# Optimization experiments

Hardware: AMD Instinct MI355X
Metric: run time of the kernel (lower is better)

## Reference

```python
import jax, jax.numpy as jnp
import numpy as np

H = 2048
N = 2_097_152
BINS = 256


def _tensor2image(x):
    # de-normalize from [-1,1]-style to [0,1] (SCGAN's tensor2image)
    return x * 0.5 + 0.5


def _cdf(vals):
    # torch.histc(vals, bins=256, min=0, max=256): unit-width bins; values here lie in [0,256)
    b = jnp.clip(jnp.floor(vals), 0, BINS - 1).astype(jnp.int32)
    hist = jnp.zeros((BINS,), jnp.float32).at[b].add(1.0)
    c = jnp.cumsum(hist)
    return c / c[BINS - 1]


def _trans_table(ref_cdf, adj_cdf):
    # table[i] = first j in 1..255 with adj[j-1] <= ref[i] <= adj[j]; else i. table[0]=0, table[255]=255.
    r = ref_cdf[:, None]                # [256,1]
    lo = adj_cdf[None, :-1]             # adj[j-1], j=1..255
    hi = adj_cdf[None, 1:]              # adj[j]
    cond = (lo <= r) & (r <= hi)        # [256,255]
    found = jnp.any(cond, axis=1)
    j_first = 1 + jnp.argmax(cond, axis=1)
    table = jnp.where(found, j_first, jnp.arange(BINS))
    table = table.at[0].set(0).at[BINS - 1].set(BINS - 1)
    return table


def _histogram_matching(dst_img, ref_img, i0, i1, i2, i3):
    dst_align = dst_img[:, i0, i1]      # [3,N]
    ref_align = ref_img[:, i2, i3]      # [3,N]
    cdf_dst = jax.vmap(_cdf)(dst_align)           # [3,256]
    cdf_ref = jax.vmap(_cdf)(ref_align)           # [3,256]
    tables = jax.vmap(_trans_table)(cdf_dst, cdf_ref)  # [3,256] int
    ix = jnp.clip(jnp.floor(dst_align), 0, BINS - 1).astype(jnp.int32)
    matched = jnp.take_along_axis(tables, ix, axis=1).astype(dst_img.dtype)  # [3,N]
    return dst_img.at[:, i0, i1].set(matched)


def setup_inputs() -> dict:
    key = jax.random.key(0)
    ks = jax.random.split(key, 9)
    return {
        "input_data": jax.random.uniform(ks[0], (1, 3, H, H), jnp.float32),
        "target_data": jax.random.uniform(ks[1], (1, 3, H, H), jnp.float32),
        "mask_src": jax.random.randint(ks[2], (1, 1, H, H), 0, 2).astype(jnp.float32),
        "mask_tar": jax.random.randint(ks[3], (1, 1, H, H), 0, 2).astype(jnp.float32),
        "idx0": jax.random.randint(ks[4], (N,), 0, H),
        "idx1": jax.random.randint(ks[5], (N,), 0, H),
        "idx2": jax.random.randint(ks[6], (N,), 0, H),
        "idx3": jax.random.randint(ks[7], (N,), 0, H),
        "ref": jax.random.uniform(ks[8], (1, 3, H, H), jnp.float32),
    }


def reference(input_data, target_data, mask_src, mask_tar, idx0, idx1, idx2, idx3, ref):
    img = _tensor2image(input_data)[0] * 255.0   # [3,H,H]
    tgt = _tensor2image(target_data)[0] * 255.0  # [3,H,H]
    rf = _tensor2image(ref)[0] * 255.0           # [3,H,H]
    m_src = jnp.broadcast_to(mask_src[0, 0], img.shape)
    m_tar = jnp.broadcast_to(mask_tar[0, 0], tgt.shape)
    input_masked = img * m_src
    target_masked = tgt * m_tar
    ref_masked = rf * m_src
    match = jax.lax.stop_gradient(
        _histogram_matching(ref_masked, target_masked, idx0, idx1, idx2, idx3)
    ) * m_src
    return jnp.mean(jnp.abs(input_masked - match))
```

## Files before the change

kernel.cpp:

```cpp
#include <hip/hip_runtime.h>

#define H 2048
#define HH (H * H)
#define NIDX 2097152
#define BINS 256
#define CH 3

#define NLIST 128
#define CAPG  139264
#define WS_HIST_DST 0
#define WS_HIST_REF 3072
#define WS_TABLE    6144
#define WS_ACC      9216
#define WS_CURS     9728
#define WS_DONE_G   10240
#define WS_DONE_L   10244
#define WS_CTRL_BYTES 16384
#define WS_SEL      16384
#define WS_ZERO_BYTES (16384 + (size_t)HH)
#define WS_BPS      (16384 + (size_t)HH)
#define WS_BPR      (WS_BPS + (size_t)HH * 4)
#define WS_LIST     (WS_BPR + (size_t)HH * 4)
#define WS_MAIN_BYTES (WS_LIST + (size_t)NLIST * CAPG * 2)

#define FB_CNT_DST  16384
#define FB_BINPACK  (16384 + (size_t)HH * 2)
#define FB_ZERO_BYTES (16384 + (size_t)HH * 2)

__device__ __forceinline__ int bin_of(float v) {
    int b = (int)floorf(v);
    return min(max(b, 0), BINS - 1);
}



#define P1_BLOCKS 512
#define P1_SPB (NIDX / P1_BLOCKS)
#define P1_CAP 96
#define PREP_BLOCKS 1024
#define PQ (HH / 4 / 4)
#define FUSE_GRID (P1_BLOCKS + PREP_BLOCKS)

__global__ __launch_bounds__(256) void prep_part_kernel(
    const float* __restrict__ mask_src, const float* __restrict__ mask_tar,
    const float* __restrict__ refimg, const float* __restrict__ tgtimg,
    unsigned int* __restrict__ bps, unsigned int* __restrict__ bpr,
    const int* __restrict__ idx0, const int* __restrict__ idx1,
    const int* __restrict__ idx2, const int* __restrict__ idx3,
    unsigned short* __restrict__ list_g, unsigned int* __restrict__ curs)
{
    __shared__ unsigned short stage[NLIST * P1_CAP];
    __shared__ unsigned int lcnt[NLIST];
    __shared__ unsigned int lbase[NLIST];

    if (blockIdx.x < P1_BLOCKS) {
        for (int i = threadIdx.x; i < NLIST; i += 256) lcnt[i] = 0u;
        __syncthreads();

        const int base4 = blockIdx.x * (P1_SPB / 4);
        #pragma unroll
        for (int r = 0; r < P1_SPB / 1024; ++r) {
            int k4 = base4 + r * 256 + threadIdx.x;
            int4 a = ((const int4*)idx0)[k4];
            int4 b = ((const int4*)idx1)[k4];
            int4 c = ((const int4*)idx2)[k4];
            int4 d = ((const int4*)idx3)[k4];
            const int pd[4] = { a.x * H + b.x, a.y * H + b.y,
                                a.z * H + b.z, a.w * H + b.w };
            const int pr[4] = { c.x * H + d.x, c.y * H + d.y,
                                c.z * H + d.z, c.w * H + d.w };
            #pragma unroll
            for (int e = 0; e < 4; ++e) {
                {
                    int l = pd[e] >> 16;
                    unsigned int pos = atomicAdd(&lcnt[l], 1u);
                    if (pos < P1_CAP) stage[l * P1_CAP + pos] = (unsigned short)(pd[e] & 0xFFFF);
                    else {
                        unsigned int g = atomicAdd(&curs[l], 1u);
                        if (g < CAPG) list_g[(size_t)l * CAPG + g] = (unsigned short)(pd[e] & 0xFFFF);
                    }
                }
                {
                    int l = 64 + (pr[e] >> 16);
                    unsigned int pos = atomicAdd(&lcnt[l], 1u);
                    if (pos < P1_CAP) stage[l * P1_CAP + pos] = (unsigned short)(pr[e] & 0xFFFF);
                    else {
                        unsigned int g = atomicAdd(&curs[l], 1u);
                        if (g < CAPG) list_g[(size_t)l * CAPG + g] = (unsigned short)(pr[e] & 0xFFFF);
                    }
                }
            }
        }
        __syncthreads();
        if (threadIdx.x < NLIST) {
            unsigned int n = min(lcnt[threadIdx.x], (unsigned int)P1_CAP);
            lbase[threadIdx.x] = atomicAdd(&curs[threadIdx.x], n);
        }
        __syncthreads();
        for (int b = 0; b < NLIST; ++b) {
            int n = (int)min(lcnt[b], (unsigned int)P1_CAP);
            unsigned int gb = lbase[b];
            for (int e = threadIdx.x; e < n; e += 256) {
                unsigned int gi = gb + e;
                if (gi < CAPG) list_g[(size_t)b * CAPG + gi] = stage[b * P1_CAP + e];
            }
        }
    } else {
        const int t = (int)(blockIdx.x - P1_BLOCKS) * 256 + threadIdx.x;
        float4 msv[4], mtv[4];
        #pragma unroll
        for (int k = 0; k < 4; ++k) {
            msv[k] = ((const float4*)mask_src)[t + k * PQ];
            mtv[k] = ((const float4*)mask_tar)[t + k * PQ];
        }
        unsigned int wsrc[4][4] = {{0u,0u,0u,0u},{0u,0u,0u,0u},{0u,0u,0u,0u},{0u,0u,0u,0u}};
        unsigned int wref[4][4] = {{0u,0u,0u,0u},{0u,0u,0u,0u},{0u,0u,0u,0u},{0u,0u,0u,0u}};
        #pragma unroll
        for (int c = 0; c < CH; ++c) {
            float4 rv[4], tv[4];
            #pragma unroll
            for (int k = 0; k < 4; ++k) {
                rv[k] = ((const float4*)(refimg + (size_t)c * HH))[t + k * PQ];
                tv[k] = ((const float4*)(tgtimg + (size_t)c * HH))[t + k * PQ];
            }
            #pragma unroll
            for (int k = 0; k < 4; ++k) {
                const float* rr = &rv[k].x;
                const float* tt = &tv[k].x;
                const float* mm = &msv[k].x;
                const float* mt2 = &mtv[k].x;
                #pragma unroll
                for (int e = 0; e < 4; ++e) {
                    float vs = (rr[e] * 0.5f + 0.5f) * 255.0f * mm[e];
                    float vt = (tt[e] * 0.5f + 0.5f) * 255.0f * mt2[e];
                    wsrc[k][e] |= ((unsigned int)bin_of(vs)) << (8 * c);
                    wref[k][e] |= ((unsigned int)bin_of(vt)) << (8 * c);
                }
            }
        }
        #pragma unroll
        for (int k = 0; k < 4; ++k) {
            uint4 os = { wsrc[k][0], wsrc[k][1], wsrc[k][2], wsrc[k][3] };
            uint4 orf = { wref[k][0], wref[k][1], wref[k][2], wref[k][3] };
            ((uint4*)bps)[t + k * PQ] = os;
            ((uint4*)bpr)[t + k * PQ] = orf;
        }
    }
}

#define G_BLOCKS 1024
__global__ __launch_bounds__(256) void gather_hist_kernel(
    const unsigned short* __restrict__ list_g, const unsigned int* __restrict__ curs,
    const unsigned int* __restrict__ bps, const unsigned int* __restrict__ bpr,
    unsigned char* __restrict__ selected,
    unsigned int* __restrict__ hist_dst, unsigned int* __restrict__ hist_ref,
    int* __restrict__ table, unsigned int* __restrict__ done)
{
    __shared__ unsigned int hh[CH * BINS];
    for (int i = threadIdx.x; i < CH * BINS; i += 256) hh[i] = 0u;
    __syncthreads();

    const int xcd  = blockIdx.x & 7;
    const int j    = blockIdx.x >> 3;
    const int bsl  = j & 15;
    const int sub  = j >> 4;
    const int side = bsl >> 3;
    const int bucket = xcd * 8 + (bsl & 7);
    const int l = side * 64 + bucket;
    const unsigned int pbase = ((unsigned int)bucket) << 16;
    const unsigned int* __restrict__ src = side ? bpr : bps;

    const unsigned int n = min(curs[l], (unsigned int)CAPG);
    const unsigned int chunk = (((n + 7u) >> 3) + 7u) & ~7u;
    const unsigned int s = (unsigned int)sub * chunk;
    const unsigned int e = min(s + chunk, n);
    const unsigned short* lbase = list_g + (size_t)l * CAPG;

    unsigned int zc = 0;
    for (unsigned int ib = s + (unsigned int)threadIdx.x * 8u; ib < e; ib += 2048u) {
        unsigned int w[8];
        unsigned int pcnt;
        if (ib + 8u <= e) {
            uint4 raw = *(const uint4*)(lbase + ib);
            const unsigned int ent[8] = {
                raw.x & 0xFFFFu, raw.x >> 16, raw.y & 0xFFFFu, raw.y >> 16,
                raw.z & 0xFFFFu, raw.z >> 16, raw.w & 0xFFFFu, raw.w >> 16 };
            #pragma unroll
            for (int k = 0; k < 8; ++k) {
                unsigned int p = pbase | ent[k];
                w[k] = src[p];
                if (side == 0) selected[p] = 1;
            }
            pcnt = 8u;
        } else {
            pcnt = e - ib;
            #pragma unroll
            for (int k = 0; k < 8; ++k) {
                if ((unsigned int)k < pcnt) {
                    unsigned int p = pbase | (unsigned int)lbase[ib + k];
                    w[k] = src[p];
                    if (side == 0) selected[p] = 1;
                } else w[k] = 0xFFFFFFFFu;
            }
        }
        #pragma unroll
        for (int k = 0; k < 8; ++k) {
            if ((unsigned int)k < pcnt) {
                unsigned int ww = w[k];
                if (ww == 0u) ++zc;
                else {
                    atomicAdd(&hh[0 * BINS + (ww & 0xFFu)], 1u);
                    atomicAdd(&hh[1 * BINS + ((ww >> 8) & 0xFFu)], 1u);
                    atomicAdd(&hh[2 * BINS + ((ww >> 16) & 0xFFu)], 1u);
                }
            }
        }
    }

    int z = (int)zc;
    #pragma unroll
    for (int off = 32; off; off >>= 1) z += __shfl_down(z, off);
    if ((threadIdx.x & 63) == 0 && z) {
        atomicAdd(&hh[0 * BINS], (unsigned int)z);
        atomicAdd(&hh[1 * BINS], (unsigned int)z);
        atomicAdd(&hh[2 * BINS], (unsigned int)z);
    }

    __syncthreads();
    unsigned int* dsthist = side ? hist_ref : hist_dst;
    for (int i = threadIdx.x; i < CH * BINS; i += 256) {
        unsigned int v = hh[i];
        if (v) atomicAdd(&dsthist[i], v);
    }

    __shared__ int is_last;
    __syncthreads();
    if (threadIdx.x == 0) {
        unsigned int t = atomicAdd(done, 1u);
        is_last = (t == gridDim.x - 1u) ? 1 : 0;
    }
    __syncthreads();
    if (!is_last) return;

    __shared__ float cd[CH * BINS];
    __shared__ float cr[CH * BINS];
    __shared__ float wpart[4];
    const int i = threadIdx.x;
    const int lane = i & 63;
    const int wave = i >> 6;

    for (int a = 0; a < 6; ++a) {
        unsigned int* h = (a < 3) ? (hist_dst + a * BINS) : (hist_ref + (a - 3) * BINS);
        float* out = (a < 3) ? (cd + a * BINS) : (cr + (a - 3) * BINS);
        float x = (float)atomicAdd(&h[i], 0u);
        #pragma unroll
        for (int off = 1; off < 64; off <<= 1) {
            float y = __shfl_up(x, off);
            if (lane >= off) x += y;
        }
        if (lane == 63) wpart[wave] = x;
        __syncthreads();
        float prefix = 0.0f;
        #pragma unroll
        for (int w = 0; w < 3; ++w) if (w < wave) prefix += wpart[w];
        x += prefix;
        float tot = wpart[0] + wpart[1] + wpart[2] + wpart[3];
        out[i] = x / tot;
        __syncthreads();
    }

    #pragma unroll
    for (int c = 0; c < CH; ++c) {
        int t;
        if (i == 0) t = 0;
        else if (i == BINS - 1) t = BINS - 1;
        else {
            float r = cd[c * BINS + i];
            int lo = 1, hi = BINS - 1;
            while (lo < hi) {
                int mid = (lo + hi) >> 1;
                if (cr[c * BINS + mid] < r) lo = mid + 1; else hi = mid;
            }
            t = (cr[c * BINS + lo - 1] <= r) ? lo : i;
        }
        table[c * BINS + i] = t;
    }
}

#define L_BLOCKS 1024
__global__ __launch_bounds__(256) void loss_sel_kernel(
    const float* __restrict__ input, const float* __restrict__ refimg,
    const float* __restrict__ mask_src, const unsigned char* __restrict__ selected,
    const int* __restrict__ table, double* __restrict__ acc,
    float* __restrict__ out_loss, unsigned int* __restrict__ done)
{
    __shared__ int tab[CH * BINS];
    for (int i = threadIdx.x; i < CH * BINS; i += 256) tab[i] = table[i];
    __syncthreads();

    const int t = blockIdx.x * 256 + threadIdx.x;
    float4 mv[4];
    uchar4 sv[4];
    #pragma unroll
    for (int k = 0; k < 4; ++k) {
        mv[k] = ((const float4*)mask_src)[t + k * PQ];
        sv[k] = ((const uchar4*)selected)[t + k * PQ];
    }

    float lsum = 0.0f;
    #pragma unroll
    for (int c = 0; c < CH; ++c) {
        float4 av4[4], rv4[4];
        #pragma unroll
        for (int k = 0; k < 4; ++k) {
            av4[k] = ((const float4*)(input  + (size_t)c * HH))[t + k * PQ];
            rv4[k] = ((const float4*)(refimg + (size_t)c * HH))[t + k * PQ];
        }
        #pragma unroll
        for (int k = 0; k < 4; ++k) {
            const float* aa = &av4[k].x;
            const float* rr = &rv4[k].x;
            const float* mm = &mv[k].x;
            const unsigned char ss[4] = { sv[k].x, sv[k].y, sv[k].z, sv[k].w };
            #pragma unroll
            for (int e = 0; e < 4; ++e) {
                float m = mm[e];
                float av = (aa[e] * 0.5f + 0.5f) * 255.0f * m;
                float rv = (rr[e] * 0.5f + 0.5f) * 255.0f * m;
                float tv = (float)tab[c * BINS + bin_of(rv)];
                float mvv = m * (ss[e] ? tv : rv);
                lsum += fabsf(av - mvv);
            }
        }
    }

    double d = (double)lsum;
    #pragma unroll
    for (int off = 32; off; off >>= 1) d += __shfl_down(d, off);
    __shared__ double wsum[4];
    int wid = threadIdx.x >> 6;
    int lane = threadIdx.x & 63;
    if (lane == 0) wsum[wid] = d;
    __syncthreads();
    if (threadIdx.x == 0) {
        double tt = wsum[0] + wsum[1] + wsum[2] + wsum[3];
        atomicAdd(acc, tt);
    }

    __shared__ int is_last;
    __syncthreads();
    if (threadIdx.x == 0) {
        unsigned int tk = atomicAdd(done, 1u);
        is_last = (tk == gridDim.x - 1u) ? 1 : 0;
    }
    __syncthreads();
    if (!is_last) return;
    if (threadIdx.x == 0) {
        double a = atomicAdd(acc, 0.0);
        out_loss[0] = (float)(a / (double)(CH * (double)HH));
    }
}

__global__ __launch_bounds__(256) void table_kernel(
    const unsigned int* __restrict__ hist_dst,
    const unsigned int* __restrict__ hist_ref,
    int* __restrict__ table)
{
    __shared__ float cd[CH * BINS];
    __shared__ float cr[CH * BINS];
    __shared__ float wpart[4];
    const int i = threadIdx.x;
    const int lane = i & 63;
    const int wave = i >> 6;

    for (int a = 0; a < 6; ++a) {
        const unsigned int* h = (a < 3) ? (hist_dst + a * BINS) : (hist_ref + (a - 3) * BINS);
        float* out = (a < 3) ? (cd + a * BINS) : (cr + (a - 3) * BINS);
        float x = (float)h[i];
        #pragma unroll
        for (int off = 1; off < 64; off <<= 1) {
            float y = __shfl_up(x, off);
            if (lane >= off) x += y;
        }
        if (lane == 63) wpart[wave] = x;
        __syncthreads();
        float prefix = 0.0f;
        #pragma unroll
        for (int w = 0; w < 3; ++w) if (w < wave) prefix += wpart[w];
        x += prefix;
        float tot = wpart[0] + wpart[1] + wpart[2] + wpart[3];
        out[i] = x / tot;
        __syncthreads();
    }

    #pragma unroll
    for (int c = 0; c < CH; ++c) {
        int t;
        if (i == 0) t = 0;
        else if (i == BINS - 1) t = BINS - 1;
        else {
            float r = cd[c * BINS + i];
            int lo = 1, hi = BINS - 1;
            while (lo < hi) {
                int mid = (lo + hi) >> 1;
                if (cr[c * BINS + mid] < r) lo = mid + 1; else hi = mid;
            }
            t = (cr[c * BINS + lo - 1] <= r) ? lo : i;
        }
        table[c * BINS + i] = t;
    }
}

__global__ void finalize_kernel(const double* __restrict__ acc, float* __restrict__ out)
{
    if (threadIdx.x == 0 && blockIdx.x == 0) {
        out[0] = (float)(acc[0] / (double)(CH * (double)HH));
    }
}


__device__ __forceinline__ void cnt_inc(unsigned int* cnt, int p) {
    atomicAdd(&cnt[p >> 1], (p & 1) ? 0x10000u : 1u);
}

__global__ __launch_bounds__(256) void fb_prep_kernel(
    const float* __restrict__ mask_tar, const float* __restrict__ tgtimg,
    unsigned int* __restrict__ binpack)
{
    const int nq = HH / 4;
    const int stride = gridDim.x * 256;
    for (int q = blockIdx.x * 256 + threadIdx.x; q < nq; q += stride) {
        float4 m4 = ((const float4*)mask_tar)[q];
        const float mm[4] = { m4.x, m4.y, m4.z, m4.w };
        unsigned int w[4] = { 0u, 0u, 0u, 0u };
        #pragma unroll
        for (int c = 0; c < CH; ++c) {
            float4 t4 = ((const float4*)(tgtimg + (size_t)c * HH))[q];
            const float tt[4] = { t4.x, t4.y, t4.z, t4.w };
            #pragma unroll
            for (int e = 0; e < 4; ++e) {
                float v = (tt[e] * 0.5f + 0.5f) * 255.0f * mm[e];
                w[e] |= ((unsigned int)bin_of(v)) << (8 * c);
            }
        }
        uint4 out = { w[0], w[1], w[2], w[3] };
        ((uint4*)binpack)[q] = out;
    }
}

__global__ __launch_bounds__(256) void fb_scatter_kernel(
    const int4* __restrict__ idx0, const int4* __restrict__ idx1,
    const int4* __restrict__ idx2, const int4* __restrict__ idx3,
    const unsigned int* __restrict__ binpack,
    unsigned int* __restrict__ cnt_dst, unsigned int* __restrict__ hist_ref)
{
    __shared__ unsigned int hr[CH * BINS];
    for (int i = threadIdx.x; i < CH * BINS; i += 256) hr[i] = 0u;
    __syncthreads();

    unsigned int zc = 0;
    const int n4 = NIDX / 4;
    const int stride = gridDim.x * 256;
    for (int k = blockIdx.x * 256 + threadIdx.x; k < n4; k += stride) {
        int4 a = idx0[k], b = idx1[k], c = idx2[k], d = idx3[k];
        int p0 = c.x * H + d.x, p1 = c.y * H + d.y;
        int p2 = c.z * H + d.z, p3 = c.w * H + d.w;
        unsigned int w0 = binpack[p0], w1 = binpack[p1];
        unsigned int w2 = binpack[p2], w3 = binpack[p3];

        cnt_inc(cnt_dst, a.x * H + b.x);
        cnt_inc(cnt_dst, a.y * H + b.y);
        cnt_inc(cnt_dst, a.z * H + b.z);
        cnt_inc(cnt_dst, a.w * H + b.w);

        const unsigned int ws2[4] = { w0, w1, w2, w3 };
        #pragma unroll
        for (int e = 0; e < 4; ++e) {
            unsigned int w = ws2[e];
            if (w == 0u) ++zc;
            else {
                atomicAdd(&hr[0 * BINS + (w & 0xFFu)], 1u);
                atomicAdd(&hr[1 * BINS + ((w >> 8) & 0xFFu)], 1u);
                atomicAdd(&hr[2 * BINS + ((w >> 16) & 0xFFu)], 1u);
            }
        }
    }

    int z = (int)zc;
    #pragma unroll
    for (int off = 32; off; off >>= 1) z += __shfl_down(z, off);
    if ((threadIdx.x & 63) == 0 && z) {
        atomicAdd(&hr[0 * BINS], (unsigned int)z);
        atomicAdd(&hr[1 * BINS], (unsigned int)z);
        atomicAdd(&hr[2 * BINS], (unsigned int)z);
    }

    __syncthreads();
    for (int i = threadIdx.x; i < CH * BINS; i += 256) {
        unsigned int v = hr[i];
        if (v) atomicAdd(&hist_ref[i], v);
    }
}

__global__ __launch_bounds__(256) void fb_sweep_kernel(
    const float* __restrict__ mask_src, const float* __restrict__ refimg,
    const unsigned int* __restrict__ cnt_dst,
    unsigned int* __restrict__ hist_dst)
{
    __shared__ unsigned int hd[CH * BINS];
    for (int i = threadIdx.x; i < CH * BINS; i += 256) hd[i] = 0u;
    __syncthreads();

    unsigned int zc = 0;
    const int nq = HH / 4;
    const int stride = gridDim.x * 256;
    for (int q = blockIdx.x * 256 + threadIdx.x; q < nq; q += stride) {
        uint2 wd = ((const uint2*)cnt_dst)[q];
        unsigned int cdc[4] = { wd.x & 0xFFFFu, wd.x >> 16, wd.y & 0xFFFFu, wd.y >> 16 };
        float4 ms4 = ((const float4*)mask_src)[q];
        const float ms[4] = { ms4.x, ms4.y, ms4.z, ms4.w };

        float rv[CH][4];
        #pragma unroll
        for (int c = 0; c < CH; ++c) {
            float4 r4 = ((const float4*)(refimg + (size_t)c * HH))[q];
            rv[c][0] = r4.x; rv[c][1] = r4.y; rv[c][2] = r4.z; rv[c][3] = r4.w;
        }
        #pragma unroll
        for (int e = 0; e < 4; ++e) {
            if (cdc[e]) {
                if (ms[e] == 0.0f) zc += cdc[e];
                else {
                    #pragma unroll
                    for (int c = 0; c < CH; ++c) {
                        float v = (rv[c][e] * 0.5f + 0.5f) * 255.0f;
                        atomicAdd(&hd[c * BINS + bin_of(v)], cdc[e]);
                    }
                }
            }
        }
    }

    int z = (int)zc;
    #pragma unroll
    for (int off = 32; off; off >>= 1) z += __shfl_down(z, off);
    if ((threadIdx.x & 63) == 0 && z) {
        atomicAdd(&hd[0 * BINS], (unsigned int)z);
        atomicAdd(&hd[1 * BINS], (unsigned int)z);
        atomicAdd(&hd[2 * BINS], (unsigned int)z);
    }

    __syncthreads();
    for (int i = threadIdx.x; i < CH * BINS; i += 256) {
        unsigned int v = hd[i];
        if (v) atomicAdd(&hist_dst[i], v);
    }
}

__global__ __launch_bounds__(256) void fb_loss_kernel(
    const float* __restrict__ input, const float* __restrict__ refimg,
    const float* __restrict__ mask_src, const unsigned int* __restrict__ cnt_dst,
    const int* __restrict__ table, double* __restrict__ acc)
{
    __shared__ int tab[CH * BINS];
    for (int i = threadIdx.x; i < CH * BINS; i += 256) tab[i] = table[i];
    __syncthreads();

    float lsum = 0.0f;
    const int nq = HH / 4;
    const int stride = gridDim.x * 256;
    for (int q = blockIdx.x * 256 + threadIdx.x; q < nq; q += stride) {
        float4 m4 = ((const float4*)mask_src)[q];
        uint2 w = ((const uint2*)cnt_dst)[q];
        const unsigned int sel[4] = { w.x & 0xFFFFu, w.x >> 16, w.y & 0xFFFFu, w.y >> 16 };
        const float mm[4] = { m4.x, m4.y, m4.z, m4.w };
        #pragma unroll
        for (int c = 0; c < CH; ++c) {
            float4 a4 = ((const float4*)(input + (size_t)c * HH))[q];
            float4 r4 = ((const float4*)(refimg + (size_t)c * HH))[q];
            const float aa[4] = { a4.x, a4.y, a4.z, a4.w };
            const float rr[4] = { r4.x, r4.y, r4.z, r4.w };
            #pragma unroll
            for (int e = 0; e < 4; ++e) {
                float m = mm[e];
                float av = (aa[e] * 0.5f + 0.5f) * 255.0f * m;
                float rv = (rr[e] * 0.5f + 0.5f) * 255.0f * m;
                float tv = (float)tab[c * BINS + bin_of(rv)];
                float mv = m * (sel[e] ? tv : rv);
                lsum += fabsf(av - mv);
            }
        }
    }

    double d = (double)lsum;
    #pragma unroll
    for (int off = 32; off; off >>= 1) d += __shfl_down(d, off);
    __shared__ double wsum[4];
    int wid = threadIdx.x >> 6;
    int lane = threadIdx.x & 63;
    if (lane == 0) wsum[wid] = d;
    __syncthreads();
    if (threadIdx.x == 0) {
        double t = wsum[0] + wsum[1] + wsum[2] + wsum[3];
        atomicAdd(acc, t);
    }
}


extern "C" void kernel_launch(void* const* d_in, const int* in_sizes, int n_in,
                              void* d_out, int out_size, void* d_ws, size_t ws_size,
                              hipStream_t stream)
{
    const float* input    = (const float*)d_in[0];
    const float* target   = (const float*)d_in[1];
    const float* mask_src = (const float*)d_in[2];
    const float* mask_tar = (const float*)d_in[3];
    const int*   idx0     = (const int*)d_in[4];
    const int*   idx1     = (const int*)d_in[5];
    const int*   idx2     = (const int*)d_in[6];
    const int*   idx3     = (const int*)d_in[7];
    const float* refimg   = (const float*)d_in[8];

    char* ws = (char*)d_ws;
    unsigned int* hist_dst = (unsigned int*)(ws + WS_HIST_DST);
    unsigned int* hist_ref = (unsigned int*)(ws + WS_HIST_REF);
    int*          table    = (int*)(ws + WS_TABLE);
    double*       acc      = (double*)(ws + WS_ACC);

    if (ws_size >= WS_MAIN_BYTES) {
        unsigned int*   curs     = (unsigned int*)(ws + WS_CURS);
        unsigned int*   done_g   = (unsigned int*)(ws + WS_DONE_G);
        unsigned int*   done_l   = (unsigned int*)(ws + WS_DONE_L);
        unsigned char*  selected = (unsigned char*)(ws + WS_SEL);
        unsigned int*   bps      = (unsigned int*)(ws + WS_BPS);
        unsigned int*   bpr      = (unsigned int*)(ws + WS_BPR);
        unsigned short* list_g   = (unsigned short*)(ws + WS_LIST);

        hipMemsetAsync(d_ws, 0, WS_ZERO_BYTES, stream);
        prep_part_kernel<<<FUSE_GRID, 256, 0, stream>>>(
            mask_src, mask_tar, refimg, target, bps, bpr,
            idx0, idx1, idx2, idx3, list_g, curs);
        gather_hist_kernel<<<G_BLOCKS, 256, 0, stream>>>(list_g, curs, bps, bpr,
                                                         selected, hist_dst, hist_ref,
                                                         table, done_g);
        loss_sel_kernel<<<L_BLOCKS, 256, 0, stream>>>(input, refimg, mask_src,
                                                      selected, table, acc,
                                                      (float*)d_out, done_l);
    } else {
        unsigned int* cnt_dst = (unsigned int*)(ws + FB_CNT_DST);
        unsigned int* binpack = (unsigned int*)(ws + FB_BINPACK);

        hipMemsetAsync(d_ws, 0, FB_ZERO_BYTES, stream);
        fb_prep_kernel<<<2048, 256, 0, stream>>>(mask_tar, target, binpack);
        fb_scatter_kernel<<<2048, 256, 0, stream>>>((const int4*)idx0, (const int4*)idx1,
                                                    (const int4*)idx2, (const int4*)idx3,
                                                    binpack, cnt_dst, hist_ref);
        fb_sweep_kernel<<<1024, 256, 0, stream>>>(mask_src, refimg, cnt_dst, hist_dst);
        table_kernel<<<1, 256, 0, stream>>>(hist_dst, hist_ref, table);
        fb_loss_kernel<<<2048, 256, 0, stream>>>(input, refimg, mask_src, cnt_dst,
                                                 table, acc);
        finalize_kernel<<<1, 64, 0, stream>>>(acc, (float*)d_out);
    }
}
```

Before: 296.5 us.

## Replace bucket partitioning with packed index arrays and XCD-filtered redundant scan

Drops the atomic-based bucket partitioning of gather indices into per-region lists. The first kernel now only packs the (row, col) index pairs into flat linear offsets. The gather kernel then has every XCD group scan all packed indices and keep only those whose address falls in its eighth of the image, which keeps bps/bpr gathers L2-local per XCD. This removes the LDS and global atomics and the staging-list writes, at the cost of each index array being read eight times instead of once.

```diff
diff --git a/kernel.cpp b/kernel.cpp
--- a/kernel.cpp
+++ b/kernel.cpp
@@ -6,13 +6,10 @@
 #define BINS 256
 #define CH 3
 
-#define NLIST 128
-#define CAPG  139264
 #define WS_HIST_DST 0
 #define WS_HIST_REF 3072
 #define WS_TABLE    6144
 #define WS_ACC      9216
-#define WS_CURS     9728
 #define WS_DONE_G   10240
 #define WS_DONE_L   10244
 #define WS_CTRL_BYTES 16384
@@ -20,8 +17,9 @@
 #define WS_ZERO_BYTES (16384 + (size_t)HH)
 #define WS_BPS      (16384 + (size_t)HH)
 #define WS_BPR      (WS_BPS + (size_t)HH * 4)
-#define WS_LIST     (WS_BPR + (size_t)HH * 4)
-#define WS_MAIN_BYTES (WS_LIST + (size_t)NLIST * CAPG * 2)
+#define WS_PD       (WS_BPR + (size_t)HH * 4)
+#define WS_PR       (WS_PD + (size_t)NIDX * 4)
+#define WS_MAIN_BYTES (WS_PR + (size_t)NIDX * 4)
 
 #define FB_CNT_DST  16384
 #define FB_BINPACK  (16384 + (size_t)HH * 2)
@@ -33,80 +31,37 @@
 }
 
 
-
-#define P1_BLOCKS 512
-#define P1_SPB (NIDX / P1_BLOCKS)
-#define P1_CAP 96
+#define PACK_BLOCKS 256
 #define PREP_BLOCKS 1024
 #define PQ (HH / 4 / 4)
-#define FUSE_GRID (P1_BLOCKS + PREP_BLOCKS)
-
-__global__ __launch_bounds__(256) void prep_part_kernel(
+#define GRID1 (PACK_BLOCKS + PREP_BLOCKS)
+
+__global__ __launch_bounds__(256) void prep_pack_kernel(
     const float* __restrict__ mask_src, const float* __restrict__ mask_tar,
     const float* __restrict__ refimg, const float* __restrict__ tgtimg,
     unsigned int* __restrict__ bps, unsigned int* __restrict__ bpr,
     const int* __restrict__ idx0, const int* __restrict__ idx1,
     const int* __restrict__ idx2, const int* __restrict__ idx3,
-    unsigned short* __restrict__ list_g, unsigned int* __restrict__ curs)
-{
-    __shared__ unsigned short stage[NLIST * P1_CAP];
-    __shared__ unsigned int lcnt[NLIST];
-    __shared__ unsigned int lbase[NLIST];
-
-    if (blockIdx.x < P1_BLOCKS) {
-        for (int i = threadIdx.x; i < NLIST; i += 256) lcnt[i] = 0u;
-        __syncthreads();
-
-        const int base4 = blockIdx.x * (P1_SPB / 4);
-        #pragma unroll
-        for (int r = 0; r < P1_SPB / 1024; ++r) {
+    unsigned int* __restrict__ pd, unsigned int* __restrict__ pr)
+{
+    if (blockIdx.x < PACK_BLOCKS) {
+        const int base4 = blockIdx.x * 2048;
+        #pragma unroll
+        for (int r = 0; r < 8; ++r) {
             int k4 = base4 + r * 256 + threadIdx.x;
             int4 a = ((const int4*)idx0)[k4];
             int4 b = ((const int4*)idx1)[k4];
             int4 c = ((const int4*)idx2)[k4];
             int4 d = ((const int4*)idx3)[k4];
-            const int pd[4] = { a.x * H + b.x, a.y * H + b.y,
-                                a.z * H + b.z, a.w * H + b.w };
-            const int pr[4] = { c.x * H + d.x, c.y * H + d.y,
-                                c.z * H + d.z, c.w * H + d.w };
-            #pragma unroll
-            for (int e = 0; e < 4; ++e) {
-                {
-                    int l = pd[e] >> 16;
-                    unsigned int pos = atomicAdd(&lcnt[l], 1u);
-                    if (pos < P1_CAP) stage[l * P1_CAP + pos] = (unsigned short)(pd[e] & 0xFFFF);
-                    else {
-                        unsigned int g = atomicAdd(&curs[l], 1u);
-                        if (g < CAPG) list_g[(size_t)l * CAPG + g] = (unsigned short)(pd[e] & 0xFFFF);
-                    }
-                }
-                {
-                    int l = 64 + (pr[e] >> 16);
-                    unsigned int pos = atomicAdd(&lcnt[l], 1u);
-                    if (pos < P1_CAP) stage[l * P1_CAP + pos] = (unsigned short)(pr[e] & 0xFFFF);
-                    else {
-                        unsigned int g = atomicAdd(&curs[l], 1u);
-                        if (g < CAPG) list_g[(size_t)l * CAPG + g] = (unsigned short)(pr[e] & 0xFFFF);
-                    }
-                }
-            }
-        }
-        __syncthreads();
-        if (threadIdx.x < NLIST) {
-            unsigned int n = min(lcnt[threadIdx.x], (unsigned int)P1_CAP);
-            lbase[threadIdx.x] = atomicAdd(&curs[threadIdx.x], n);
-        }
-        __syncthreads();
-        for (int b = 0; b < NLIST; ++b) {
-            int n = (int)min(lcnt[b], (unsigned int)P1_CAP);
-            unsigned int gb = lbase[b];
-            for (int e = threadIdx.x; e < n; e += 256) {
-                unsigned int gi = gb + e;
-                if (gi < CAPG) list_g[(size_t)b * CAPG + gi] = stage[b * P1_CAP + e];
-            }
+            uint4 opd = { (unsigned int)(a.x * H + b.x), (unsigned int)(a.y * H + b.y),
+                          (unsigned int)(a.z * H + b.z), (unsigned int)(a.w * H + b.w) };
+            uint4 opr = { (unsigned int)(c.x * H + d.x), (unsigned int)(c.y * H + d.y),
+                          (unsigned int)(c.z * H + d.z), (unsigned int)(c.w * H + d.w) };
+            ((uint4*)pd)[k4] = opd;
+            ((uint4*)pr)[k4] = opr;
         }
     } else {
-        const int t = (int)(blockIdx.x - P1_BLOCKS) * 256 + threadIdx.x;
+        const int t = (int)(blockIdx.x - PACK_BLOCKS) * 256 + threadIdx.x;
         float4 msv[4], mtv[4];
         #pragma unroll
         for (int k = 0; k < 4; ++k) {
@@ -148,89 +103,81 @@
     }
 }
 
-#define G_BLOCKS 1024
-__global__ __launch_bounds__(256) void gather_hist_kernel(
-    const unsigned short* __restrict__ list_g, const unsigned int* __restrict__ curs,
+#define SG_BLOCKS 1024
+__global__ __launch_bounds__(256) void scan_gather_kernel(
+    const unsigned int* __restrict__ pd, const unsigned int* __restrict__ pr,
     const unsigned int* __restrict__ bps, const unsigned int* __restrict__ bpr,
     unsigned char* __restrict__ selected,
     unsigned int* __restrict__ hist_dst, unsigned int* __restrict__ hist_ref,
     int* __restrict__ table, unsigned int* __restrict__ done)
 {
-    __shared__ unsigned int hh[CH * BINS];
-    for (int i = threadIdx.x; i < CH * BINS; i += 256) hh[i] = 0u;
-    __syncthreads();
-
-    const int xcd  = blockIdx.x & 7;
-    const int j    = blockIdx.x >> 3;
-    const int bsl  = j & 15;
-    const int sub  = j >> 4;
-    const int side = bsl >> 3;
-    const int bucket = xcd * 8 + (bsl & 7);
-    const int l = side * 64 + bucket;
-    const unsigned int pbase = ((unsigned int)bucket) << 16;
-    const unsigned int* __restrict__ src = side ? bpr : bps;
-
-    const unsigned int n = min(curs[l], (unsigned int)CAPG);
-    const unsigned int chunk = (((n + 7u) >> 3) + 7u) & ~7u;
-    const unsigned int s = (unsigned int)sub * chunk;
-    const unsigned int e = min(s + chunk, n);
-    const unsigned short* lbase = list_g + (size_t)l * CAPG;
-
-    unsigned int zc = 0;
-    for (unsigned int ib = s + (unsigned int)threadIdx.x * 8u; ib < e; ib += 2048u) {
-        unsigned int w[8];
-        unsigned int pcnt;
-        if (ib + 8u <= e) {
-            uint4 raw = *(const uint4*)(lbase + ib);
-            const unsigned int ent[8] = {
-                raw.x & 0xFFFFu, raw.x >> 16, raw.y & 0xFFFFu, raw.y >> 16,
-                raw.z & 0xFFFFu, raw.z >> 16, raw.w & 0xFFFFu, raw.w >> 16 };
-            #pragma unroll
-            for (int k = 0; k < 8; ++k) {
-                unsigned int p = pbase | ent[k];
-                w[k] = src[p];
-                if (side == 0) selected[p] = 1;
-            }
-            pcnt = 8u;
-        } else {
-            pcnt = e - ib;
-            #pragma unroll
-            for (int k = 0; k < 8; ++k) {
-                if ((unsigned int)k < pcnt) {
-                    unsigned int p = pbase | (unsigned int)lbase[ib + k];
-                    w[k] = src[p];
-                    if (side == 0) selected[p] = 1;
-                } else w[k] = 0xFFFFFFFFu;
-            }
-        }
-        #pragma unroll
-        for (int k = 0; k < 8; ++k) {
-            if ((unsigned int)k < pcnt) {
-                unsigned int ww = w[k];
-                if (ww == 0u) ++zc;
+    __shared__ unsigned int hd[CH * BINS];
+    __shared__ unsigned int hr[CH * BINS];
+    for (int i = threadIdx.x; i < CH * BINS; i += 256) { hd[i] = 0u; hr[i] = 0u; }
+    __syncthreads();
+
+    const unsigned int xcd = (unsigned int)(blockIdx.x & 7);
+    const int slot = blockIdx.x >> 3;
+    const int base4 = slot * 4096;
+
+    unsigned int zc_d = 0, zc_r = 0;
+    for (int r = 0; r < 16; ++r) {
+        int k4 = base4 + r * 256 + threadIdx.x;
+        uint4 pdv = ((const uint4*)pd)[k4];
+        uint4 prv = ((const uint4*)pr)[k4];
+        const unsigned int PD[4] = { pdv.x, pdv.y, pdv.z, pdv.w };
+        const unsigned int PR[4] = { prv.x, prv.y, prv.z, prv.w };
+        #pragma unroll
+        for (int e = 0; e < 4; ++e) {
+            unsigned int p = PD[e];
+            if ((p >> 19) == xcd) {
+                unsigned int w = bps[p];
+                selected[p] = 1;
+                if (w == 0u) ++zc_d;
                 else {
-                    atomicAdd(&hh[0 * BINS + (ww & 0xFFu)], 1u);
-                    atomicAdd(&hh[1 * BINS + ((ww >> 8) & 0xFFu)], 1u);
-                    atomicAdd(&hh[2 * BINS + ((ww >> 16) & 0xFFu)], 1u);
+                    atomicAdd(&hd[0 * BINS + (w & 0xFFu)], 1u);
+                    atomicAdd(&hd[1 * BINS + ((w >> 8) & 0xFFu)], 1u);
+                    atomicAdd(&hd[2 * BINS + ((w >> 16) & 0xFFu)], 1u);
                 }
             }
         }
-    }
-
-    int z = (int)zc;
-    #pragma unroll
-    for (int off = 32; off; off >>= 1) z += __shfl_down(z, off);
-    if ((threadIdx.x & 63) == 0 && z) {
-        atomicAdd(&hh[0 * BINS], (unsigned int)z);
-        atomicAdd(&hh[1 * BINS], (unsigned int)z);
-        atomicAdd(&hh[2 * BINS], (unsigned int)z);
-    }
-
-    __syncthreads();
-    unsigned int* dsthist = side ? hist_ref : hist_dst;
+        #pragma unroll
+        for (int e = 0; e < 4; ++e) {
+            unsigned int p = PR[e];
+            if ((p >> 19) == xcd) {
+                unsigned int w = bpr[p];
+                if (w == 0u) ++zc_r;
+                else {
+                    atomicAdd(&hr[0 * BINS + (w & 0xFFu)], 1u);
+                    atomicAdd(&hr[1 * BINS + ((w >> 8) & 0xFFu)], 1u);
+                    atomicAdd(&hr[2 * BINS + ((w >> 16) & 0xFFu)], 1u);
+                }
+            }
+        }
+    }
+
+    int zd = (int)zc_d, zr = (int)zc_r;
+    #pragma unroll
+    for (int off = 32; off; off >>= 1) { zd += __shfl_down(zd, off); zr += __shfl_down(zr, off); }
+    if ((threadIdx.x & 63) == 0) {
+        if (zd) {
+            atomicAdd(&hd[0 * BINS], (unsigned int)zd);
+            atomicAdd(&hd[1 * BINS], (unsigned int)zd);
+            atomicAdd(&hd[2 * BINS], (unsigned int)zd);
+        }
+        if (zr) {
+            atomicAdd(&hr[0 * BINS], (unsigned int)zr);
+            atomicAdd(&hr[1 * BINS], (unsigned int)zr);
+            atomicAdd(&hr[2 * BINS], (unsigned int)zr);
+        }
+    }
+
+    __syncthreads();
     for (int i = threadIdx.x; i < CH * BINS; i += 256) {
-        unsigned int v = hh[i];
-        if (v) atomicAdd(&dsthist[i], v);
+        unsigned int v = hd[i];
+        if (v) atomicAdd(&hist_dst[i], v);
+        v = hr[i];
+        if (v) atomicAdd(&hist_ref[i], v);
     }
 
     __shared__ int is_last;
@@ -628,21 +575,21 @@
     double*       acc      = (double*)(ws + WS_ACC);
 
     if (ws_size >= WS_MAIN_BYTES) {
-        unsigned int*   curs     = (unsigned int*)(ws + WS_CURS);
         unsigned int*   done_g   = (unsigned int*)(ws + WS_DONE_G);
         unsigned int*   done_l   = (unsigned int*)(ws + WS_DONE_L);
         unsigned char*  selected = (unsigned char*)(ws + WS_SEL);
         unsigned int*   bps      = (unsigned int*)(ws + WS_BPS);
         unsigned int*   bpr      = (unsigned int*)(ws + WS_BPR);
-        unsigned short* list_g   = (unsigned short*)(ws + WS_LIST);
+        unsigned int*   pd       = (unsigned int*)(ws + WS_PD);
+        unsigned int*   pr       = (unsigned int*)(ws + WS_PR);
 
         hipMemsetAsync(d_ws, 0, WS_ZERO_BYTES, stream);
-        prep_part_kernel<<<FUSE_GRID, 256, 0, stream>>>(
+        prep_pack_kernel<<<GRID1, 256, 0, stream>>>(
             mask_src, mask_tar, refimg, target, bps, bpr,
-            idx0, idx1, idx2, idx3, list_g, curs);
-        gather_hist_kernel<<<G_BLOCKS, 256, 0, stream>>>(list_g, curs, bps, bpr,
-                                                         selected, hist_dst, hist_ref,
-                                                         table, done_g);
+            idx0, idx1, idx2, idx3, pd, pr);
+        scan_gather_kernel<<<SG_BLOCKS, 256, 0, stream>>>(pd, pr, bps, bpr,
+                                                          selected, hist_dst, hist_ref,
+                                                          table, done_g);
         loss_sel_kernel<<<L_BLOCKS, 256, 0, stream>>>(input, refimg, mask_src,
                                                       selected, table, acc,
                                                       (float*)d_out, done_l);
```

After: 339.4 us. 1.14x slower.
